# Optimization experiments

Measured on AMD Instinct MI355X. Metric: run time of the kernel, lower is better.

Reference implementation:

```python
import jax, jax.numpy as jnp
import numpy as np

C_IN, C_OUT, GROUPS = 1024, 1024, 8
H, W_SP = 256, 256


def _block_diag_mask():
    # group-conv sparsity pattern: block-diagonal [C_out, C_in] boolean mask
    blk = jnp.ones((C_OUT // GROUPS, C_IN // GROUPS), dtype=jnp.float32)
    return jnp.kron(jnp.eye(GROUPS, dtype=jnp.float32), blk) > 0


def setup_inputs() -> dict:
    key = jax.random.key(0)
    k1, k2 = jax.random.split(key)
    x = jax.random.normal(k1, (1, C_IN, H, W_SP), dtype=jnp.float32)
    W = jax.random.normal(k2, (C_OUT, C_IN), dtype=jnp.float32)
    mask = _block_diag_mask()  # constant sparsity pattern (nnz = C_in*C_out/groups)
    return {"x": x, "W": W, "mask": mask}


def reference(x, W, mask):
    # SparseGroupConv2d.forward: y = sparse_W @ x.view(C_in, H*W), viewed back
    h, w = x.shape[2], x.shape[3]
    x_ = x.reshape(C_IN, h * w)                      # [C_in, P]
    W_sp = jnp.where(mask, W, 0.0)                   # masked weight == sparse COO values
    y_ = jnp.matmul(W_sp, x_)                        # [C_out, P]
    return y_.reshape(1, C_OUT, h, w)
```

## Files before the change

kernel.cpp:

```cpp
#include <hip/hip_runtime.h>
#include <hip/hip_bf16.h>


#define GC   128
#define CIN  1024
#define PT   65536
#define BN   128
#define XLD  132

typedef __attribute__((ext_vector_type(8))) short bf16x8;
typedef __attribute__((ext_vector_type(4))) float f32x4;

__device__ __forceinline__ unsigned short f2bf(float f) {
    union { float f; unsigned int u; } v; v.f = f;
    unsigned int r = v.u + 0x7FFF + ((v.u >> 16) & 1);
    return (unsigned short)(r >> 16);
}

__global__ __launch_bounds__(256) void sparse_group_conv_kernel(
        const float* __restrict__ x, const float* __restrict__ w,
        float* __restrict__ y) {
    __shared__ unsigned short Wlds[GC * GC];
    __shared__ unsigned short Xlds[GC * XLD];

    const int t  = threadIdx.x;
    const int g  = blockIdx.y;
    const int p0 = blockIdx.x * BN;

    const float* Xg = x + (size_t)(g * GC) * PT + p0;
    const float* Wg = w + (size_t)(g * GC) * CIN + g * GC;

    float4 xr[16];
    #pragma unroll
    for (int it = 0; it < 16; ++it) {
        const int f = it * 256 + t;
        const int row = f >> 5;
        const int m = f & 31;
        xr[it] = *reinterpret_cast<const float4*>(Xg + (size_t)row * PT + 4 * m);
    }
    float4 wr[16];
    #pragma unroll
    for (int it = 0; it < 16; ++it) {
        const int mm = it * 8 + (t >> 5);
        wr[it] = *reinterpret_cast<const float4*>(Wg + (size_t)mm * CIN + (t & 31) * 4);
    }

    #pragma unroll
    for (int it = 0; it < 16; ++it) {
        const int f = it * 256 + t;
        const int row = f >> 5;
        const int m = f & 31;
        ushort4 h;
        h.x = f2bf(xr[it].x); h.y = f2bf(xr[it].y);
        h.z = f2bf(xr[it].z); h.w = f2bf(xr[it].w);
        *reinterpret_cast<ushort4*>(&Xlds[row * XLD + 4 * m]) = h;
    }
    #pragma unroll
    for (int it = 0; it < 16; ++it) {
        const int mm = it * 8 + (t >> 5);
        const int k = (t & 31) * 4;
        ushort4 h;
        h.x = f2bf(wr[it].x); h.y = f2bf(wr[it].y);
        h.z = f2bf(wr[it].z); h.w = f2bf(wr[it].w);
        const int idx = (mm * GC + k) ^ ((mm & 7) << 3);
        *reinterpret_cast<ushort4*>(&Wlds[idx]) = h;
    }
    __syncthreads();

    const int lane = t & 63;
    const int wv   = t >> 6;
    const int r    = lane & 15;
    const int q    = lane >> 4;

    f32x4 acc[2][8];
    #pragma unroll
    for (int pg = 0; pg < 2; ++pg)
        #pragma unroll
        for (int mi = 0; mi < 8; ++mi)
            acc[pg][mi] = (f32x4){0.f, 0.f, 0.f, 0.f};

    #pragma unroll
    for (int ks = 0; ks < 4; ++ks) {
        bf16x8 b[2];
        #pragma unroll
        for (int pg = 0; pg < 2; ++pg) {
            const int px = wv * 32 + pg * 16 + r;
            const unsigned short* col = &Xlds[(ks * 32 + q * 8) * XLD + px];
            short tmp[8];
            #pragma unroll
            for (int j = 0; j < 8; ++j) tmp[j] = (short)col[j * XLD];
            b[pg] = (bf16x8){tmp[0], tmp[1], tmp[2], tmp[3],
                             tmp[4], tmp[5], tmp[6], tmp[7]};
        }
        #pragma unroll
        for (int mi = 0; mi < 8; ++mi) {
            const int mrow = mi * 16 + r;
            const int idx = (mrow * GC + ks * 32 + q * 8) ^ ((mrow & 7) << 3);
            const bf16x8 a = *reinterpret_cast<const bf16x8*>(&Wlds[idx]);
            acc[0][mi] = __builtin_amdgcn_mfma_f32_16x16x32_bf16(a, b[0], acc[0][mi], 0, 0, 0);
            acc[1][mi] = __builtin_amdgcn_mfma_f32_16x16x32_bf16(a, b[1], acc[1][mi], 0, 0, 0);
        }
    }

    float* Yg = y + (size_t)(g * GC) * PT + p0;
    #pragma unroll
    for (int pg = 0; pg < 2; ++pg) {
        float* yp = Yg + wv * 32 + pg * 16 + r;
        #pragma unroll
        for (int mi = 0; mi < 8; ++mi) {
            #pragma unroll
            for (int rr = 0; rr < 4; ++rr) {
                yp[(size_t)(mi * 16 + q * 4 + rr) * PT] = acc[pg][mi][rr];
            }
        }
    }
}

extern "C" void kernel_launch(void* const* d_in, const int* in_sizes, int n_in,
                              void* d_out, int out_size, void* d_ws, size_t ws_size,
                              hipStream_t stream) {
    const float* x = (const float*)d_in[0];
    const float* w = (const float*)d_in[1];
    float* y = (float*)d_out;

    dim3 grid(PT / BN, 8);
    dim3 block(256);
    sparse_group_conv_kernel<<<grid, block, 0, stream>>>(x, w, y);
}
```

Baseline: 456.5 us.

## Pre-pack weights into MFMA fragment layout and read them from global/L2

Adds a small prep kernel that converts each group's diagonal weight block to bf16 and lays it out in per-lane MFMA fragment order in the workspace. The main kernel drops the weight LDS tile and its fp32 loads and conversion, and instead reads the A fragments straight from global memory, which should hit in L2 since they are shared across blocks. It also sets launch bounds for 4 blocks per CU, which the smaller LDS footprint allows. The cost is an extra kernel launch plus global-latency loads inside the MFMA loop.

```diff
diff --git a/kernel.cpp b/kernel.cpp
--- a/kernel.cpp
+++ b/kernel.cpp
@@ -7,6 +7,7 @@
 #define PT   65536
 #define BN   128
 #define XLD  132
+#define WFRAG_PER_G (4 * 8 * 64 * 8)
 
 typedef __attribute__((ext_vector_type(8))) short bf16x8;
 typedef __attribute__((ext_vector_type(4))) float f32x4;
@@ -17,10 +18,32 @@
     return (unsigned short)(r >> 16);
 }
 
-__global__ __launch_bounds__(256) void sparse_group_conv_kernel(
-        const float* __restrict__ x, const float* __restrict__ w,
+__global__ __launch_bounds__(256) void wprep_kernel(
+        const float* __restrict__ w, unsigned short* __restrict__ wf) {
+    const int g = blockIdx.x;
+    const int t = threadIdx.x;
+    #pragma unroll
+    for (int i = 0; i < 8; ++i) {
+        const int id   = i * 256 + t;
+        const int f    = id >> 6;
+        const int lane = id & 63;
+        const int mi = f & 7, ks = f >> 3;
+        const int row = g * GC + mi * 16 + (lane & 15);
+        const int col = g * GC + ks * 32 + (lane >> 4) * 8;
+        const float4 w0 = *reinterpret_cast<const float4*>(w + (size_t)row * CIN + col);
+        const float4 w1 = *reinterpret_cast<const float4*>(w + (size_t)row * CIN + col + 4);
+        ushort4 h0, h1;
+        h0.x = f2bf(w0.x); h0.y = f2bf(w0.y); h0.z = f2bf(w0.z); h0.w = f2bf(w0.w);
+        h1.x = f2bf(w1.x); h1.y = f2bf(w1.y); h1.z = f2bf(w1.z); h1.w = f2bf(w1.w);
+        unsigned short* dst = wf + (size_t)g * WFRAG_PER_G + (size_t)id * 8;
+        *reinterpret_cast<ushort4*>(dst)     = h0;
+        *reinterpret_cast<ushort4*>(dst + 4) = h1;
+    }
+}
+
+__global__ __launch_bounds__(256, 4) void sparse_group_conv_kernel(
+        const float* __restrict__ x, const unsigned short* __restrict__ wf,
         float* __restrict__ y) {
-    __shared__ unsigned short Wlds[GC * GC];
     __shared__ unsigned short Xlds[GC * XLD];
 
     const int t  = threadIdx.x;
@@ -28,42 +51,24 @@
     const int p0 = blockIdx.x * BN;
 
     const float* Xg = x + (size_t)(g * GC) * PT + p0;
-    const float* Wg = w + (size_t)(g * GC) * CIN + g * GC;
 
     float4 xr[16];
     #pragma unroll
     for (int it = 0; it < 16; ++it) {
-        const int f = it * 256 + t;
-        const int row = f >> 5;
-        const int m = f & 31;
+        const int f_i = it * 256 + t;
+        const int row = f_i >> 5;
+        const int m   = f_i & 31;
         xr[it] = *reinterpret_cast<const float4*>(Xg + (size_t)row * PT + 4 * m);
     }
-    float4 wr[16];
     #pragma unroll
     for (int it = 0; it < 16; ++it) {
-        const int mm = it * 8 + (t >> 5);
-        wr[it] = *reinterpret_cast<const float4*>(Wg + (size_t)mm * CIN + (t & 31) * 4);
-    }
-
-    #pragma unroll
-    for (int it = 0; it < 16; ++it) {
-        const int f = it * 256 + t;
-        const int row = f >> 5;
-        const int m = f & 31;
+        const int f_i = it * 256 + t;
+        const int row = f_i >> 5;
+        const int m   = f_i & 31;
         ushort4 h;
         h.x = f2bf(xr[it].x); h.y = f2bf(xr[it].y);
         h.z = f2bf(xr[it].z); h.w = f2bf(xr[it].w);
         *reinterpret_cast<ushort4*>(&Xlds[row * XLD + 4 * m]) = h;
-    }
-    #pragma unroll
-    for (int it = 0; it < 16; ++it) {
-        const int mm = it * 8 + (t >> 5);
-        const int k = (t & 31) * 4;
-        ushort4 h;
-        h.x = f2bf(wr[it].x); h.y = f2bf(wr[it].y);
-        h.z = f2bf(wr[it].z); h.w = f2bf(wr[it].w);
-        const int idx = (mm * GC + k) ^ ((mm & 7) << 3);
-        *reinterpret_cast<ushort4*>(&Wlds[idx]) = h;
     }
     __syncthreads();
 
@@ -71,6 +76,8 @@
     const int wv   = t >> 6;
     const int r    = lane & 15;
     const int q    = lane >> 4;
+
+    const unsigned short* wg = wf + (size_t)g * WFRAG_PER_G + (size_t)lane * 8;
 
     f32x4 acc[2][8];
     #pragma unroll
@@ -94,9 +101,8 @@
         }
         #pragma unroll
         for (int mi = 0; mi < 8; ++mi) {
-            const int mrow = mi * 16 + r;
-            const int idx = (mrow * GC + ks * 32 + q * 8) ^ ((mrow & 7) << 3);
-            const bf16x8 a = *reinterpret_cast<const bf16x8*>(&Wlds[idx]);
+            const bf16x8 a = *reinterpret_cast<const bf16x8*>(
+                wg + (size_t)((ks * 8 + mi) * 64) * 8);
             acc[0][mi] = __builtin_amdgcn_mfma_f32_16x16x32_bf16(a, b[0], acc[0][mi], 0, 0, 0);
             acc[1][mi] = __builtin_amdgcn_mfma_f32_16x16x32_bf16(a, b[1], acc[1][mi], 0, 0, 0);
         }
@@ -122,8 +128,9 @@
     const float* x = (const float*)d_in[0];
     const float* w = (const float*)d_in[1];
     float* y = (float*)d_out;
+    unsigned short* wf = (unsigned short*)d_ws;
 
+    wprep_kernel<<<dim3(8), dim3(256), 0, stream>>>(w, wf);
     dim3 grid(PT / BN, 8);
-    dim3 block(256);
-    sparse_group_conv_kernel<<<grid, block, 0, stream>>>(x, w, y);
+    sparse_group_conv_kernel<<<grid, dim3(256), 0, stream>>>(x, wf, y);
 }
```

After: 468.1 us. 1.03x slower.
